# Optimization experiments

Hardware: AMD Instinct MI355X
Metric: run time of the kernel (lower is better)

## Reference

```python
import jax, jax.numpy as jnp
import numpy as np

N = 8192
D = 512
INSTANCES = 8  # samples per class (balanced PK batch)
ALPHA = 40.0
BASE = 0.5
BIG = 1e9  # finite sentinel instead of inf (safe under vjp)


def setup_inputs() -> dict:
    key = jax.random.key(0)
    emb = jax.random.normal(key, (N, D), dtype=jnp.float32)
    emb = emb / jnp.linalg.norm(emb, axis=1, keepdims=True)  # unit-norm embeddings
    label = jnp.arange(N, dtype=jnp.int64) // INSTANCES       # balanced classes
    return {"embedding": emb, "label": label}


def reference(embedding, label):
    n = embedding.shape[0]
    sim = embedding @ embedding.T                      # [n, n]
    same = label[:, None] == label[None, :]
    eye = jnp.eye(n, dtype=bool)
    pos_mask = same & ~eye                             # positives, excl. self
    neg_mask = ~same                                   # negatives

    # per-row hard-mining thresholds (sampling_method == 1)
    max_pos = jnp.max(jnp.where(pos_mask, sim, -BIG), axis=1)  # pos_pair_[-1]
    min_neg = jnp.min(jnp.where(neg_mask, sim, BIG), axis=1)   # neg_pair_[0]

    neg_sel = neg_mask & (sim < max_pos[:, None])
    pos_sel = pos_mask & (sim > min_neg[:, None])

    pos_cnt = jnp.sum(pos_sel, axis=1)
    neg_cnt = jnp.sum(neg_sel, axis=1)

    # pos_loss_i = mean(1 - pos_pair) if any selected else 0
    pos_sum = jnp.sum(jnp.where(pos_sel, 1.0 - sim, 0.0), axis=1)
    pos_loss = jnp.where(pos_cnt > 0, pos_sum / jnp.maximum(pos_cnt, 1), 0.0)

    # neg_loss_i = (2/alpha)*log(1 + sum exp(alpha*(neg_pair - base))) + mean(neg_pair)
    exp_sum = jnp.sum(jnp.where(neg_sel, jnp.exp(ALPHA * (sim - BASE)), 0.0), axis=1)
    neg_mean = jnp.sum(jnp.where(neg_sel, sim, 0.0), axis=1) / jnp.maximum(neg_cnt, 1)
    neg_loss = jnp.where(neg_cnt > 0, (2.0 / ALPHA) * jnp.log1p(exp_sum) + neg_mean, 0.0)

    loss = jnp.sum(pos_loss + neg_loss) / n
    triplets = jnp.sum(neg_cnt // 2)                   # self.triplets accumulator
    return loss, triplets, 0
```

## Files before the change

kernel.cpp:

```cpp
#include <hip/hip_runtime.h>

typedef float f32x4 __attribute__((ext_vector_type(4)));
typedef short s16x8 __attribute__((ext_vector_type(8)));

#define NROWS 8192
#define DIM   512
#define ALPHA 40.0f
#define BASEV 0.5f
#define BIGF  1e9f
#define NPANEL 64
#define NPAIRS 2080
#define NSLOT  64

#define OFF_HI   0ull
#define OFF_LO   (OFF_HI + (unsigned long long)NROWS*DIM*2)
#define OFF_MAXP (OFF_LO + (unsigned long long)NROWS*DIM*2)
#define OFF_SBLK (OFF_MAXP + (unsigned long long)NROWS*4)
#define OFF_PMIN (OFF_SBLK + 1024ull*64*4)
#define OFF_PCNT (OFF_PMIN + (unsigned long long)NSLOT*NROWS*4)
#define OFF_PSUM (OFF_PCNT + (unsigned long long)NSLOT*NROWS*4)
#define OFF_PEXP (OFF_PSUM + (unsigned long long)NSLOT*NROWS*4)
#define OFF_RLOSS (OFF_PEXP + (unsigned long long)NSLOT*NROWS*4)
#define OFF_RTRIP (OFF_RLOSS + (unsigned long long)NROWS*4)

__device__ inline unsigned short bf16rne(float x) {
    unsigned u = __float_as_uint(x);
    unsigned r = (u + 0x7FFFu + ((u >> 16) & 1u)) >> 16;
    return (unsigned short)r;
}

__global__ __launch_bounds__(256) void k_prep(const float* __restrict__ emb,
                                              uint4* __restrict__ hi, uint4* __restrict__ lo) {
    int tid = blockIdx.x * 256 + threadIdx.x;
    int row = tid & (NROWS - 1);
    int chunk = tid >> 13;
    const float4* s4 = (const float4*)(emb + row * DIM + chunk * 8);
    float4 x0 = s4[0], x1 = s4[1];
    float xs[8] = {x0.x, x0.y, x0.z, x0.w, x1.x, x1.y, x1.z, x1.w};
    unsigned hw[4], lw[4];
#pragma unroll
    for (int p = 0; p < 4; ++p) {
        unsigned short h0 = bf16rne(xs[2 * p]);
        unsigned short h1 = bf16rne(xs[2 * p + 1]);
        float hf0 = __uint_as_float(((unsigned)h0) << 16);
        float hf1 = __uint_as_float(((unsigned)h1) << 16);
        unsigned short l0 = bf16rne(xs[2 * p] - hf0);
        unsigned short l1 = bf16rne(xs[2 * p + 1] - hf1);
        hw[p] = (unsigned)h0 | ((unsigned)h1 << 16);
        lw[p] = (unsigned)l0 | ((unsigned)l1 << 16);
    }
    uint4 H = {hw[0], hw[1], hw[2], hw[3]};
    uint4 L = {lw[0], lw[1], lw[2], lw[3]};
    hi[chunk * NROWS + row] = H;
    lo[chunk * NROWS + row] = L;
}

__global__ __launch_bounds__(64) void k_gram(const float* __restrict__ emb,
                                             float* __restrict__ simblk,
                                             float* __restrict__ maxpos) {
    __shared__ float A[8 * 516];
    int cls = blockIdx.x, t = threadIdx.x;
    const float* base = emb + (size_t)cls * 8 * DIM;
    for (int it = 0; it < 64; ++it) {
        int idx = t + 64 * it;
        int r = idx >> 9, k = idx & 511;
        A[r * 516 + k] = base[idx];
    }
    __syncthreads();
    int i = t >> 3, j = t & 7;
    const float* ai = A + i * 516;
    const float* aj = A + j * 516;
    float s = 0.f;
    for (int k = 0; k < 512; ++k) s += ai[k] * aj[k];
    simblk[cls * 64 + t] = s;
    float m = (i == j) ? -BIGF : s;
#pragma unroll
    for (int off = 1; off < 8; off <<= 1) m = fmaxf(m, __shfl_xor(m, off, 64));
    if (j == 0) maxpos[cls * 8 + i] = m;
}

__global__ __launch_bounds__(256, 2) void k_main(const unsigned short* __restrict__ ehi,
                                                 const unsigned short* __restrict__ elo,
                                                 const float* __restrict__ maxpos,
                                                 float* __restrict__ pmin,
                                                 unsigned* __restrict__ pcnt,
                                                 float* __restrict__ psum,
                                                 float* __restrict__ pexp) {
    __shared__ float sMaxA[128], sMaxB[128];
    __shared__ float rMin[2][128];
    __shared__ unsigned rCnt[2][128];
    __shared__ float rSum[2][128], rExp[2][128];
    __shared__ float cMin[2][128];
    __shared__ unsigned cCnt[2][128];
    __shared__ float cSum[2][128], cExp[2][128];

    int t = threadIdx.x;
    int lane = t & 63;
    int w = t >> 6;
    int wr = w >> 1, wc = w & 1;

    int bid = blockIdx.x;
    int wg = (bid & 7) * 260 + (bid >> 3);
    int J = (int)((sqrtf(8.0f * (float)wg + 1.0f) - 1.0f) * 0.5f);
    while ((J + 1) * (J + 2) / 2 <= wg) ++J;
    while (J * (J + 1) / 2 > wg) --J;
    int I = wg - J * (J + 1) / 2;
    int r0 = I * 128, c0 = J * 128;
    bool diag = (I == J);

    if (t < 128) sMaxA[t] = maxpos[r0 + t];
    else sMaxB[t - 128] = maxpos[c0 + (t - 128)];

    int rl = (lane >> 4) * 4;
    int ri = lane & 15;
    int cg = lane >> 4;

    int arow = r0 + wr * 64 + ri;
    int brow = c0 + wc * 64 + ri;
    const s16x8* Ehi = (const s16x8*)ehi;
    const s16x8* Elo = (const s16x8*)elo;

    f32x4 acc[4][4];
#pragma unroll
    for (int m = 0; m < 4; ++m)
#pragma unroll
        for (int n = 0; n < 4; ++n) acc[m][n] = (f32x4){0.f, 0.f, 0.f, 0.f};

    auto load_set = [&](int kt, s16x8 aH[4], s16x8 aL[4], s16x8 bH[4], s16x8 bL[4]) {
        size_t kb = (size_t)(kt * 4 + cg) * NROWS;
        const s16x8* pAh = Ehi + kb + arow;
        const s16x8* pAl = Elo + kb + arow;
        const s16x8* pBh = Ehi + kb + brow;
        const s16x8* pBl = Elo + kb + brow;
#pragma unroll
        for (int m = 0; m < 4; ++m) { aH[m] = pAh[m * 16]; aL[m] = pAl[m * 16]; }
#pragma unroll
        for (int n = 0; n < 4; ++n) { bH[n] = pBh[n * 16]; bL[n] = pBl[n * 16]; }
    };

    auto mfma_set = [&](const s16x8 aH[4], const s16x8 aL[4],
                        const s16x8 bH[4], const s16x8 bL[4]) {
#pragma unroll
        for (int m = 0; m < 4; ++m)
#pragma unroll
            for (int n = 0; n < 4; ++n) {
                acc[m][n] = __builtin_amdgcn_mfma_f32_16x16x32_bf16(aH[m], bH[n], acc[m][n], 0, 0, 0);
                acc[m][n] = __builtin_amdgcn_mfma_f32_16x16x32_bf16(aH[m], bL[n], acc[m][n], 0, 0, 0);
                acc[m][n] = __builtin_amdgcn_mfma_f32_16x16x32_bf16(aL[m], bH[n], acc[m][n], 0, 0, 0);
            }
    };

    s16x8 aH0[4], aL0[4], bH0[4], bL0[4];
    s16x8 aH1[4], aL1[4], bH1[4], bL1[4];

    load_set(0, aH0, aL0, bH0, bL0);
#pragma unroll 1
    for (int kt = 0; kt < 16; kt += 2) {
        load_set(kt + 1, aH1, aL1, bH1, bL1);
        mfma_set(aH0, aL0, bH0, bL0);
        if (kt + 2 < 16) load_set(kt + 2, aH0, aL0, bH0, bL0);
        mfma_set(aH1, aL1, bH1, bL1);
    }

    __syncthreads();

    float mxB[4];
#pragma unroll
    for (int n = 0; n < 4; ++n) mxB[n] = sMaxB[wc * 64 + n * 16 + ri];

    float cmn[4], csm[4], ces[4];
    int cct[4];
#pragma unroll
    for (int n = 0; n < 4; ++n) { cmn[n] = BIGF; csm[n] = 0.f; ces[n] = 0.f; cct[n] = 0; }

#pragma unroll
    for (int m = 0; m < 4; ++m) {
#pragma unroll
        for (int jj = 0; jj < 4; ++jj) {
            int lr0 = wr * 64 + m * 16 + rl + jj;
            int grow = r0 + lr0;
            int rcls = grow >> 3;
            float mxA = sMaxA[lr0];
            float mn = BIGF, sm = 0.f, es = 0.f;
            int ct = 0;
#pragma unroll
            for (int n = 0; n < 4; ++n) {
                float v = acc[m][n][jj];
                int gcol = c0 + wc * 64 + n * 16 + ri;
                if ((gcol >> 3) != rcls) {
                    float e = __expf(ALPHA * (v - BASEV));
                    mn = fminf(mn, v);
                    if (v < mxA) { ct++; sm += v; es += e; }
                    if (!diag) {
                        cmn[n] = fminf(cmn[n], v);
                        if (v < mxB[n]) { cct[n]++; csm[n] += v; ces[n] += e; }
                    }
                }
            }
#pragma unroll
            for (int off = 1; off < 16; off <<= 1) {
                mn = fminf(mn, __shfl_xor(mn, off, 64));
                sm += __shfl_xor(sm, off, 64);
                es += __shfl_xor(es, off, 64);
                ct += __shfl_xor(ct, off, 64);
            }
            if ((lane & 15) == 0) {
                rMin[wc][lr0] = mn;
                rCnt[wc][lr0] = (unsigned)ct;
                rSum[wc][lr0] = sm;
                rExp[wc][lr0] = es;
            }
        }
    }

    if (!diag) {
#pragma unroll
        for (int n = 0; n < 4; ++n) {
#pragma unroll
            for (int off = 16; off < 64; off <<= 1) {
                cmn[n] = fminf(cmn[n], __shfl_xor(cmn[n], off, 64));
                csm[n] += __shfl_xor(csm[n], off, 64);
                ces[n] += __shfl_xor(ces[n], off, 64);
                cct[n] += __shfl_xor(cct[n], off, 64);
            }
        }
        if (lane < 16) {
#pragma unroll
            for (int n = 0; n < 4; ++n) {
                int lc = wc * 64 + n * 16 + ri;
                cMin[wr][lc] = cmn[n];
                cCnt[wr][lc] = (unsigned)cct[n];
                cSum[wr][lc] = csm[n];
                cExp[wr][lc] = ces[n];
            }
        }
    }

    __syncthreads();
    if (t < 128) {
        int gi = J * NROWS + r0 + t;
        pmin[gi] = fminf(rMin[0][t], rMin[1][t]);
        pcnt[gi] = rCnt[0][t] + rCnt[1][t];
        psum[gi] = rSum[0][t] + rSum[1][t];
        pexp[gi] = rExp[0][t] + rExp[1][t];
    } else if (!diag) {
        int tc = t - 128;
        int gi = I * NROWS + c0 + tc;
        pmin[gi] = fminf(cMin[0][tc], cMin[1][tc]);
        pcnt[gi] = cCnt[0][tc] + cCnt[1][tc];
        psum[gi] = cSum[0][tc] + cSum[1][tc];
        pexp[gi] = cExp[0][tc] + cExp[1][tc];
    }
}

__global__ __launch_bounds__(256) void k_fin1(const float* __restrict__ pmin,
                                              const unsigned* __restrict__ pcnt,
                                              const float* __restrict__ psum,
                                              const float* __restrict__ pexp,
                                              const float* __restrict__ simblk,
                                              float* __restrict__ rowloss,
                                              unsigned* __restrict__ rowtrip) {
    int row = blockIdx.x * 256 + threadIdx.x;
    float mn = BIGF;
    unsigned ct = 0;
    float sm = 0.f, es = 0.f;
#pragma unroll 8
    for (int c = 0; c < NSLOT; ++c) {
        int gi = c * NROWS + row;
        mn = fminf(mn, pmin[gi]);
        ct += pcnt[gi];
        sm += psum[gi];
        es += pexp[gi];
    }
    int cls = row >> 3, ir = row & 7;
    const float* sb = simblk + cls * 64 + ir * 8;
    float psumv = 0.f;
    int pcntv = 0;
#pragma unroll
    for (int j = 0; j < 8; ++j) {
        if (j == ir) continue;
        float s = sb[j];
        if (s > mn) { pcntv++; psumv += 1.f - s; }
    }
    float pl = (pcntv > 0) ? psumv / (float)pcntv : 0.f;
    float nl = (ct > 0) ? (2.0f / ALPHA) * log1pf(es) + sm / (float)ct : 0.f;
    rowloss[row] = pl + nl;
    rowtrip[row] = ct >> 1;
}

__global__ __launch_bounds__(256) void k_fin2(const float* __restrict__ rowloss,
                                              const unsigned* __restrict__ rowtrip,
                                              float* __restrict__ out) {
    __shared__ float lsum[256];
    __shared__ unsigned long long ltrip[256];
    int t = threadIdx.x;
    float acc = 0.f;
    unsigned long long trip = 0ull;
    for (int it = 0; it < NROWS / 256; ++it) {
        int row = t + it * 256;
        acc += rowloss[row];
        trip += (unsigned long long)rowtrip[row];
    }
    lsum[t] = acc;
    ltrip[t] = trip;
    __syncthreads();
    for (int s = 128; s > 0; s >>= 1) {
        if (t < s) { lsum[t] += lsum[t + s]; ltrip[t] += ltrip[t + s]; }
        __syncthreads();
    }
    if (t == 0) {
        out[0] = lsum[0] / (float)NROWS;
        out[1] = (float)ltrip[0];
        out[2] = 0.f;
    }
}

extern "C" void kernel_launch(void* const* d_in, const int* in_sizes, int n_in,
                              void* d_out, int out_size, void* d_ws, size_t ws_size,
                              hipStream_t stream) {
    const float* emb = (const float*)d_in[0];
    char* ws = (char*)d_ws;
    unsigned short* ehi = (unsigned short*)(ws + OFF_HI);
    unsigned short* elo = (unsigned short*)(ws + OFF_LO);
    float* maxpos = (float*)(ws + OFF_MAXP);
    float* simblk = (float*)(ws + OFF_SBLK);
    float* pmin = (float*)(ws + OFF_PMIN);
    unsigned* pcnt = (unsigned*)(ws + OFF_PCNT);
    float* psum = (float*)(ws + OFF_PSUM);
    float* pexp = (float*)(ws + OFF_PEXP);
    float* rowloss = (float*)(ws + OFF_RLOSS);
    unsigned* rowtrip = (unsigned*)(ws + OFF_RTRIP);
    float* out = (float*)d_out;

    hipLaunchKernelGGL(k_prep, dim3(64 * NROWS / 256), dim3(256), 0, stream,
                       emb, (uint4*)ehi, (uint4*)elo);
    hipLaunchKernelGGL(k_gram, dim3(1024), dim3(64), 0, stream, emb, simblk, maxpos);
    hipLaunchKernelGGL(k_main, dim3(NPAIRS), dim3(256), 0, stream,
                       ehi, elo, maxpos, pmin, pcnt, psum, pexp);
    hipLaunchKernelGGL(k_fin1, dim3(NROWS / 256), dim3(256), 0, stream,
                       pmin, pcnt, psum, pexp, simblk, rowloss, rowtrip);
    hipLaunchKernelGGL(k_fin2, dim3(1), dim3(256), 0, stream, rowloss, rowtrip, out);
}
```

Baseline: 160.9 us.

## Stage B operand tiles into LDS via direct global-to-LDS async loads

The B-side hi/lo bf16 fragments are now fetched with global_load_lds straight into per-wave double-buffered shared memory instead of into registers. Manual vmcnt waits and a scheduling barrier pace the pipeline, and the A operands still go through registers. The aim is to cut VGPR pressure and let B loads overlap the MFMA work. In exchange it adds LDS traffic, about 64KB of shared memory per block that may limit occupancy, and fragile hand-counted waitcnt values.

```diff
diff --git a/kernel.cpp b/kernel.cpp
--- a/kernel.cpp
+++ b/kernel.cpp
@@ -86,6 +86,7 @@
                                                  unsigned* __restrict__ pcnt,
                                                  float* __restrict__ psum,
                                                  float* __restrict__ pexp) {
+    __shared__ short Bls[4][2][8 * 64 * 8];
     __shared__ float sMaxA[128], sMaxB[128];
     __shared__ float rMin[2][128];
     __shared__ unsigned rCnt[2][128];
@@ -116,9 +117,32 @@
     int cg = lane >> 4;
 
     int arow = r0 + wr * 64 + ri;
-    int brow = c0 + wc * 64 + ri;
-    const s16x8* Ehi = (const s16x8*)ehi;
-    const s16x8* Elo = (const s16x8*)elo;
+    const s16x8* pAh = (const s16x8*)ehi + (size_t)cg * NROWS + arow;
+    const s16x8* pAl = (const s16x8*)elo + (size_t)cg * NROWS + arow;
+
+    const unsigned short* pBh = ehi + (size_t)(c0 + wc * 64 + lane) * 8;
+    const unsigned short* pBl = elo + (size_t)(c0 + wc * 64 + lane) * 8;
+    short* myB = &Bls[w][0][0];
+
+    auto stageB = [&](int kt) {
+        short* dst = myB + (kt & 1) * 4096;
+#pragma unroll
+        for (int c = 0; c < 4; ++c) {
+            size_t off = (size_t)(kt * 4 + c) * (NROWS * 8);
+            __builtin_amdgcn_global_load_lds(
+                (const __attribute__((address_space(1))) void*)(pBh + off),
+                (__attribute__((address_space(3))) void*)(dst + c * 512), 16, 0, 0);
+            __builtin_amdgcn_global_load_lds(
+                (const __attribute__((address_space(1))) void*)(pBl + off),
+                (__attribute__((address_space(3))) void*)(dst + (4 + c) * 512), 16, 0, 0);
+        }
+    };
+    auto loadA = [&](int kt, s16x8 aH[4], s16x8 aL[4]) {
+        const s16x8* ph = pAh + (size_t)kt * 4 * NROWS;
+        const s16x8* pl = pAl + (size_t)kt * 4 * NROWS;
+#pragma unroll
+        for (int m = 0; m < 4; ++m) { aH[m] = ph[m * 16]; aL[m] = pl[m * 16]; }
+    };
 
     f32x4 acc[4][4];
 #pragma unroll
@@ -126,20 +150,18 @@
 #pragma unroll
         for (int n = 0; n < 4; ++n) acc[m][n] = (f32x4){0.f, 0.f, 0.f, 0.f};
 
-    auto load_set = [&](int kt, s16x8 aH[4], s16x8 aL[4], s16x8 bH[4], s16x8 bL[4]) {
-        size_t kb = (size_t)(kt * 4 + cg) * NROWS;
-        const s16x8* pAh = Ehi + kb + arow;
-        const s16x8* pAl = Elo + kb + arow;
-        const s16x8* pBh = Ehi + kb + brow;
-        const s16x8* pBl = Elo + kb + brow;
-#pragma unroll
-        for (int m = 0; m < 4; ++m) { aH[m] = pAh[m * 16]; aL[m] = pAl[m * 16]; }
-#pragma unroll
-        for (int n = 0; n < 4; ++n) { bH[n] = pBh[n * 16]; bL[n] = pBl[n * 16]; }
-    };
-
-    auto mfma_set = [&](const s16x8 aH[4], const s16x8 aL[4],
-                        const s16x8 bH[4], const s16x8 bL[4]) {
+    auto compute = [&](int kt, const s16x8 aH[4], const s16x8 aL[4]) {
+        if (kt < 15) asm volatile("s_waitcnt vmcnt(24)" ::: "memory");
+        else         asm volatile("s_waitcnt vmcnt(8)" ::: "memory");
+        __builtin_amdgcn_sched_barrier(0);
+        const short* base = myB + (kt & 1) * 4096;
+        s16x8 bH[4], bL[4];
+#pragma unroll
+        for (int n = 0; n < 4; ++n) {
+            int ro = (n * 16 + ri) * 8;
+            bH[n] = *(const s16x8*)(base + cg * 512 + ro);
+            bL[n] = *(const s16x8*)(base + (4 + cg) * 512 + ro);
+        }
 #pragma unroll
         for (int m = 0; m < 4; ++m)
 #pragma unroll
@@ -150,16 +172,19 @@
             }
     };
 
-    s16x8 aH0[4], aL0[4], bH0[4], bL0[4];
-    s16x8 aH1[4], aL1[4], bH1[4], bL1[4];
-
-    load_set(0, aH0, aL0, bH0, bL0);
+    s16x8 aH0[4], aL0[4], aH1[4], aL1[4];
+    stageB(0);
+    loadA(0, aH0, aL0);
 #pragma unroll 1
     for (int kt = 0; kt < 16; kt += 2) {
-        load_set(kt + 1, aH1, aL1, bH1, bL1);
-        mfma_set(aH0, aL0, bH0, bL0);
-        if (kt + 2 < 16) load_set(kt + 2, aH0, aL0, bH0, bL0);
-        mfma_set(aH1, aL1, bH1, bL1);
+        stageB(kt + 1);
+        loadA(kt + 1, aH1, aL1);
+        compute(kt, aH0, aL0);
+        if (kt + 2 < 16) {
+            stageB(kt + 2);
+            loadA(kt + 2, aH0, aL0);
+        }
+        compute(kt + 1, aH1, aL1);
     }
 
     __syncthreads();
```

After: 175.9 us. +9.4%, slower.

## Split k_main tile across 8 waves with smaller per-wave accumulators

Applied to the files above, without the earlier changes.

Doubles the k_main workgroup to 512 threads (8 waves), each wave now covering a 64x32 sub-tile instead of 64x64, which halves the accumulator and operand register footprint and allows more waves per CU. The manual double-buffered load/MFMA software pipeline is replaced by a plain loop with unroll 2, leaving latency hiding to occupancy and the compiler. Row partial reductions now combine four column-wave slots. Each wave reloads the A operand for a narrower B strip, so per-MFMA global load traffic rises, and less explicit prefetching may expose load latency.

```diff
diff --git a/kernel.cpp b/kernel.cpp
--- a/kernel.cpp
+++ b/kernel.cpp
@@ -79,7 +79,7 @@
     if (j == 0) maxpos[cls * 8 + i] = m;
 }
 
-__global__ __launch_bounds__(256, 2) void k_main(const unsigned short* __restrict__ ehi,
+__global__ __launch_bounds__(512, 4) void k_main(const unsigned short* __restrict__ ehi,
                                                  const unsigned short* __restrict__ elo,
                                                  const float* __restrict__ maxpos,
                                                  float* __restrict__ pmin,
@@ -87,9 +87,9 @@
                                                  float* __restrict__ psum,
                                                  float* __restrict__ pexp) {
     __shared__ float sMaxA[128], sMaxB[128];
-    __shared__ float rMin[2][128];
-    __shared__ unsigned rCnt[2][128];
-    __shared__ float rSum[2][128], rExp[2][128];
+    __shared__ float rMin[4][128];
+    __shared__ unsigned rCnt[4][128];
+    __shared__ float rSum[4][128], rExp[4][128];
     __shared__ float cMin[2][128];
     __shared__ unsigned cCnt[2][128];
     __shared__ float cSum[2][128], cExp[2][128];
@@ -97,7 +97,8 @@
     int t = threadIdx.x;
     int lane = t & 63;
     int w = t >> 6;
-    int wr = w >> 1, wc = w & 1;
+    int wr = w >> 2;
+    int wcq = w & 3;
 
     int bid = blockIdx.x;
     int wg = (bid & 7) * 260 + (bid >> 3);
@@ -109,69 +110,55 @@
     bool diag = (I == J);
 
     if (t < 128) sMaxA[t] = maxpos[r0 + t];
-    else sMaxB[t - 128] = maxpos[c0 + (t - 128)];
+    else if (t < 256) sMaxB[t - 128] = maxpos[c0 + (t - 128)];
 
     int rl = (lane >> 4) * 4;
     int ri = lane & 15;
     int cg = lane >> 4;
 
     int arow = r0 + wr * 64 + ri;
-    int brow = c0 + wc * 64 + ri;
+    int brow = c0 + wcq * 32 + ri;
     const s16x8* Ehi = (const s16x8*)ehi;
     const s16x8* Elo = (const s16x8*)elo;
 
-    f32x4 acc[4][4];
+    f32x4 acc[4][2];
 #pragma unroll
     for (int m = 0; m < 4; ++m)
 #pragma unroll
-        for (int n = 0; n < 4; ++n) acc[m][n] = (f32x4){0.f, 0.f, 0.f, 0.f};
-
-    auto load_set = [&](int kt, s16x8 aH[4], s16x8 aL[4], s16x8 bH[4], s16x8 bL[4]) {
+        for (int n = 0; n < 2; ++n) acc[m][n] = (f32x4){0.f, 0.f, 0.f, 0.f};
+
+#pragma unroll 2
+    for (int kt = 0; kt < 16; ++kt) {
         size_t kb = (size_t)(kt * 4 + cg) * NROWS;
         const s16x8* pAh = Ehi + kb + arow;
         const s16x8* pAl = Elo + kb + arow;
         const s16x8* pBh = Ehi + kb + brow;
         const s16x8* pBl = Elo + kb + brow;
+        s16x8 aH[4], aL[4], bH[2], bL[2];
 #pragma unroll
         for (int m = 0; m < 4; ++m) { aH[m] = pAh[m * 16]; aL[m] = pAl[m * 16]; }
 #pragma unroll
-        for (int n = 0; n < 4; ++n) { bH[n] = pBh[n * 16]; bL[n] = pBl[n * 16]; }
-    };
-
-    auto mfma_set = [&](const s16x8 aH[4], const s16x8 aL[4],
-                        const s16x8 bH[4], const s16x8 bL[4]) {
+        for (int n = 0; n < 2; ++n) { bH[n] = pBh[n * 16]; bL[n] = pBl[n * 16]; }
 #pragma unroll
         for (int m = 0; m < 4; ++m)
 #pragma unroll
-            for (int n = 0; n < 4; ++n) {
+            for (int n = 0; n < 2; ++n) {
                 acc[m][n] = __builtin_amdgcn_mfma_f32_16x16x32_bf16(aH[m], bH[n], acc[m][n], 0, 0, 0);
                 acc[m][n] = __builtin_amdgcn_mfma_f32_16x16x32_bf16(aH[m], bL[n], acc[m][n], 0, 0, 0);
                 acc[m][n] = __builtin_amdgcn_mfma_f32_16x16x32_bf16(aL[m], bH[n], acc[m][n], 0, 0, 0);
             }
-    };
-
-    s16x8 aH0[4], aL0[4], bH0[4], bL0[4];
-    s16x8 aH1[4], aL1[4], bH1[4], bL1[4];
-
-    load_set(0, aH0, aL0, bH0, bL0);
-#pragma unroll 1
-    for (int kt = 0; kt < 16; kt += 2) {
-        load_set(kt + 1, aH1, aL1, bH1, bL1);
-        mfma_set(aH0, aL0, bH0, bL0);
-        if (kt + 2 < 16) load_set(kt + 2, aH0, aL0, bH0, bL0);
-        mfma_set(aH1, aL1, bH1, bL1);
     }
 
     __syncthreads();
 
-    float mxB[4];
-#pragma unroll
-    for (int n = 0; n < 4; ++n) mxB[n] = sMaxB[wc * 64 + n * 16 + ri];
-
-    float cmn[4], csm[4], ces[4];
-    int cct[4];
-#pragma unroll
-    for (int n = 0; n < 4; ++n) { cmn[n] = BIGF; csm[n] = 0.f; ces[n] = 0.f; cct[n] = 0; }
+    float mxB[2];
+#pragma unroll
+    for (int n = 0; n < 2; ++n) mxB[n] = sMaxB[wcq * 32 + n * 16 + ri];
+
+    float cmn[2], csm[2], ces[2];
+    int cct[2];
+#pragma unroll
+    for (int n = 0; n < 2; ++n) { cmn[n] = BIGF; csm[n] = 0.f; ces[n] = 0.f; cct[n] = 0; }
 
 #pragma unroll
     for (int m = 0; m < 4; ++m) {
@@ -184,9 +171,9 @@
             float mn = BIGF, sm = 0.f, es = 0.f;
             int ct = 0;
 #pragma unroll
-            for (int n = 0; n < 4; ++n) {
+            for (int n = 0; n < 2; ++n) {
                 float v = acc[m][n][jj];
-                int gcol = c0 + wc * 64 + n * 16 + ri;
+                int gcol = c0 + wcq * 32 + n * 16 + ri;
                 if ((gcol >> 3) != rcls) {
                     float e = __expf(ALPHA * (v - BASEV));
                     mn = fminf(mn, v);
@@ -205,17 +192,17 @@
                 ct += __shfl_xor(ct, off, 64);
             }
             if ((lane & 15) == 0) {
-                rMin[wc][lr0] = mn;
-                rCnt[wc][lr0] = (unsigned)ct;
-                rSum[wc][lr0] = sm;
-                rExp[wc][lr0] = es;
+                rMin[wcq][lr0] = mn;
+                rCnt[wcq][lr0] = (unsigned)ct;
+                rSum[wcq][lr0] = sm;
+                rExp[wcq][lr0] = es;
             }
         }
     }
 
     if (!diag) {
 #pragma unroll
-        for (int n = 0; n < 4; ++n) {
+        for (int n = 0; n < 2; ++n) {
 #pragma unroll
             for (int off = 16; off < 64; off <<= 1) {
                 cmn[n] = fminf(cmn[n], __shfl_xor(cmn[n], off, 64));
@@ -226,8 +213,8 @@
         }
         if (lane < 16) {
 #pragma unroll
-            for (int n = 0; n < 4; ++n) {
-                int lc = wc * 64 + n * 16 + ri;
+            for (int n = 0; n < 2; ++n) {
+                int lc = wcq * 32 + n * 16 + ri;
                 cMin[wr][lc] = cmn[n];
                 cCnt[wr][lc] = (unsigned)cct[n];
                 cSum[wr][lc] = csm[n];
@@ -239,11 +226,11 @@
     __syncthreads();
     if (t < 128) {
         int gi = J * NROWS + r0 + t;
-        pmin[gi] = fminf(rMin[0][t], rMin[1][t]);
-        pcnt[gi] = rCnt[0][t] + rCnt[1][t];
-        psum[gi] = rSum[0][t] + rSum[1][t];
-        pexp[gi] = rExp[0][t] + rExp[1][t];
-    } else if (!diag) {
+        pmin[gi] = fminf(fminf(rMin[0][t], rMin[1][t]), fminf(rMin[2][t], rMin[3][t]));
+        pcnt[gi] = rCnt[0][t] + rCnt[1][t] + rCnt[2][t] + rCnt[3][t];
+        psum[gi] = ((rSum[0][t] + rSum[1][t]) + rSum[2][t]) + rSum[3][t];
+        pexp[gi] = ((rExp[0][t] + rExp[1][t]) + rExp[2][t]) + rExp[3][t];
+    } else if (t < 256 && !diag) {
         int tc = t - 128;
         int gi = I * NROWS + c0 + tc;
         pmin[gi] = fminf(cMin[0][tc], cMin[1][tc]);
@@ -335,7 +322,7 @@
     hipLaunchKernelGGL(k_prep, dim3(64 * NROWS / 256), dim3(256), 0, stream,
                        emb, (uint4*)ehi, (uint4*)elo);
     hipLaunchKernelGGL(k_gram, dim3(1024), dim3(64), 0, stream, emb, simblk, maxpos);
-    hipLaunchKernelGGL(k_main, dim3(NPAIRS), dim3(256), 0, stream,
+    hipLaunchKernelGGL(k_main, dim3(NPAIRS), dim3(512), 0, stream,
                        ehi, elo, maxpos, pmin, pcnt, psum, pexp);
     hipLaunchKernelGGL(k_fin1, dim3(NROWS / 256), dim3(256), 0, stream,
                        pmin, pcnt, psum, pexp, simblk, rowloss, rowtrip);
```

Measured after the change: 202.5 us. +25.9%, slower.
